# Kernel tuning notes

Hardware: AMD Instinct MI355X
Metric: run time of the kernel (lower is better)

Reference implementation:

```python
import jax, jax.numpy as jnp
import numpy as np

N = 50000          # num vertices
E = 20000          # num hyperedges
NNZ = 320000       # num incidences
IN_C = 256
HEADS = 8
OUT_C = 32
D = HEADS * OUT_C  # 256, projected feature dim


def setup_inputs() -> dict:
    key = jax.random.key(0)
    k1, k2, k3, k4 = jax.random.split(key, 4)
    X = jax.random.normal(k1, (N, IN_C), dtype=jnp.float32)
    vertex = jax.random.randint(k2, (NNZ,), 0, N, dtype=jnp.int64)
    edges = jax.random.randint(k3, (NNZ,), 0, E, dtype=jnp.int64)
    # Linear weight stored as [in, out] so projection is X @ W
    W = jax.random.normal(k4, (IN_C, D), dtype=jnp.float32) / np.sqrt(IN_C)
    eps = jnp.zeros((1,), dtype=jnp.float32)
    return {"X": X, "vertex": vertex, "edges": edges, "W": W, "eps": eps}


def reference(X, vertex, edges, W, eps):
    # Linear projection: [N, in] @ [in, heads*out] -> [N, D]
    Xp = X @ W
    # vertex -> edge: gather per-incidence vertex features, sum into hyperedges
    Xve = Xp[vertex]                                            # [NNZ, D]
    Xe = jax.ops.segment_sum(Xve, edges, num_segments=E)        # [E, D]
    # edge -> vertex: gather per-incidence edge features, sum into vertices
    Xev = Xe[edges]                                             # [NNZ, D]
    Xv = jax.ops.segment_sum(Xev, vertex, num_segments=N)       # [N, D]
    # GIN update
    return (1.0 + eps) * Xp + Xv
```

## Files before the change

kernel.cpp:

```cpp
#include <hip/hip_runtime.h>

constexpr int NV   = 50000;
constexpr int NE   = 20000;
constexpr int NNZI = 320000;
constexpr int KD   = 256;
constexpr int DD   = 256;
constexpr int ECAP = 64;
constexpr int VCAP = 32;

constexpr size_t alignup256(size_t x) { return (x + 255) & ~(size_t)255; }

constexpr size_t XPH_BYTES   = (size_t)NV * DD * 2;
constexpr size_t XEH_BYTES   = (size_t)NE * DD * 2;
constexpr size_t DEGV_BYTES  = alignup256((size_t)NV * sizeof(int));
constexpr size_t DEGE_BYTES  = alignup256((size_t)NE * sizeof(int));
constexpr size_t VLIST_BYTES = (size_t)NV * VCAP * sizeof(int);
constexpr size_t ELIST_BYTES = (size_t)NE * ECAP * sizeof(int);
constexpr size_t BPACK_ELEMS = 8ull * 16 * 64 * 8;
constexpr size_t BPACK_BYTES = BPACK_ELEMS * 2;

constexpr size_t XPH_OFF   = 0;
constexpr size_t XEH_OFF   = XPH_OFF + XPH_BYTES;
constexpr size_t DEGV_OFF  = XEH_OFF + XEH_BYTES;
constexpr size_t DEGE_OFF  = DEGV_OFF + DEGV_BYTES;
constexpr size_t VLIST_OFF = DEGE_OFF + DEGE_BYTES;
constexpr size_t ELIST_OFF = VLIST_OFF + VLIST_BYTES;
constexpr size_t BF_OFF    = ELIST_OFF + ELIST_BYTES;

typedef float    floatx4 __attribute__((ext_vector_type(4)));
typedef _Float16 halfx8  __attribute__((ext_vector_type(8)));
typedef _Float16 halfx4  __attribute__((ext_vector_type(4)));

__global__ __launch_bounds__(256) void pack_w(
        const float* __restrict__ W, _Float16* __restrict__ Bf) {
    const int idx  = blockIdx.x * 256 + threadIdx.x;
    const int k0   = idx >> 10;
    const int nt   = (idx >> 6) & 15;
    const int lane = idx & 63;
    const int krow = k0 * 32 + ((lane >> 4) << 3);
    const int ncol = nt * 16 + (lane & 15);
#pragma unroll
    for (int j = 0; j < 8; ++j)
        Bf[(size_t)idx * 8 + j] = (_Float16)W[(size_t)(krow + j) * DD + ncol];
}

__global__ __launch_bounds__(256) void gemm_mfma(
        const float* __restrict__ X, const _Float16* __restrict__ Bf,
        _Float16* __restrict__ Xp_h) {
    const int lane = threadIdx.x & 63;
    const int wv   = threadIdx.x >> 6;
    const int row_base = blockIdx.x * 64 + (wv >> 1) * 32;
    const int ntg0     = blockIdx.y * 8 + (wv & 1) * 4;

    floatx4 acc[2][4];
#pragma unroll
    for (int mt = 0; mt < 2; ++mt)
#pragma unroll
        for (int nt = 0; nt < 4; ++nt) acc[mt][nt] = (floatx4)0.f;

    const int lrow   = lane & 15;
    const int kgroup = (lane >> 4) << 3;

    int r0 = row_base + lrow;       if (r0 >= NV) r0 = NV - 1;
    int r1 = row_base + 16 + lrow;  if (r1 >= NV) r1 = NV - 1;
    const float* pA0 = &X[(size_t)r0 * KD + kgroup];
    const float* pA1 = &X[(size_t)r1 * KD + kgroup];

    float4 xb[2][2][2];
    halfx8 bb[2][4];

    auto loads = [&](int k0, int buf) {
        xb[buf][0][0] = *reinterpret_cast<const float4*>(pA0 + k0 * 32);
        xb[buf][0][1] = *reinterpret_cast<const float4*>(pA0 + k0 * 32 + 4);
        xb[buf][1][0] = *reinterpret_cast<const float4*>(pA1 + k0 * 32);
        xb[buf][1][1] = *reinterpret_cast<const float4*>(pA1 + k0 * 32 + 4);
#pragma unroll
        for (int nt = 0; nt < 4; ++nt) {
            const size_t boff = ((size_t)(k0 * 16 + ntg0 + nt) * 64 + lane) * 8;
            bb[buf][nt] = *reinterpret_cast<const halfx8*>(&Bf[boff]);
        }
    };

    loads(0, 0);
    for (int k0 = 0; k0 < 8; ++k0) {
        const int cur = k0 & 1;
        if (k0 < 7) loads(k0 + 1, cur ^ 1);
        halfx8 a[2];
#pragma unroll
        for (int mt = 0; mt < 2; ++mt) {
            const float* xp = reinterpret_cast<const float*>(&xb[cur][mt][0]);
#pragma unroll
            for (int j = 0; j < 8; ++j) a[mt][j] = (_Float16)xp[j];
        }
#pragma unroll
        for (int nt = 0; nt < 4; ++nt)
#pragma unroll
            for (int mt = 0; mt < 2; ++mt)
                acc[mt][nt] = __builtin_amdgcn_mfma_f32_16x16x32_f16(a[mt], bb[cur][nt], acc[mt][nt], 0, 0, 0);
    }

    const int rgroup = (lane >> 4) << 2;
#pragma unroll
    for (int mt = 0; mt < 2; ++mt) {
#pragma unroll
        for (int r = 0; r < 4; ++r) {
            const int row = row_base + mt * 16 + rgroup + r;
            if (row < NV) {
#pragma unroll
                for (int nt = 0; nt < 4; ++nt)
                    Xp_h[(size_t)row * DD + (ntg0 + nt) * 16 + (lane & 15)] =
                        (_Float16)acc[mt][nt][r];
            }
        }
    }
}

__global__ __launch_bounds__(256) void build_csr(
        const int* __restrict__ vertex, const int* __restrict__ edges,
        int* __restrict__ deg_v, int* __restrict__ deg_e,
        int* __restrict__ vlist, int* __restrict__ elist) {
    const int i = blockIdx.x * blockDim.x + threadIdx.x;
    if (i >= NNZI) return;
    const int v = vertex[i];
    const int e = edges[i];
    const int pe = atomicAdd(&deg_e[e], 1);
    if (pe < ECAP) elist[(size_t)e * ECAP + pe] = v;
    const int pv = atomicAdd(&deg_v[v], 1);
    if (pv < VCAP) vlist[(size_t)v * VCAP + pv] = e;
}

__global__ __launch_bounds__(256) void edge_gather(
        const _Float16* __restrict__ Xp_h, const int* __restrict__ deg_e,
        const int* __restrict__ elist, _Float16* __restrict__ Xe_h) {
    const int lane = threadIdx.x & 63;
    const int wid  = (blockIdx.x * blockDim.x + threadIdx.x) >> 6;
    if (wid >= NE) return;
    int cnt = deg_e[wid];
    if (cnt > ECAP) cnt = ECAP;
    const int idxl = elist[(size_t)wid * ECAP + lane];
    const int col  = lane * 4;
    float a0 = 0.f, a1 = 0.f, a2 = 0.f, a3 = 0.f;
    for (int base = 0; base < cnt; base += 8) {
#pragma unroll
        for (int jj = 0; jj < 8; ++jj) {
            const int j   = base + jj;
            const int sel = j < cnt ? j : 0;
            const float s = j < cnt ? 1.f : 0.f;
            const int v = __shfl(idxl, sel);
            const halfx4 x = *reinterpret_cast<const halfx4*>(&Xp_h[(size_t)v * DD + col]);
            a0 = fmaf(s, (float)x[0], a0);
            a1 = fmaf(s, (float)x[1], a1);
            a2 = fmaf(s, (float)x[2], a2);
            a3 = fmaf(s, (float)x[3], a3);
        }
    }
    halfx4 o;
    o[0] = (_Float16)a0; o[1] = (_Float16)a1; o[2] = (_Float16)a2; o[3] = (_Float16)a3;
    *reinterpret_cast<halfx4*>(&Xe_h[(size_t)wid * DD + col]) = o;
}

__global__ __launch_bounds__(256) void vertex_gather(
        const _Float16* __restrict__ Xp_h, const _Float16* __restrict__ Xe_h,
        const int* __restrict__ deg_v, const int* __restrict__ vlist,
        const float* __restrict__ eps, float* __restrict__ out) {
    const int lane = threadIdx.x & 63;
    const int wid  = (blockIdx.x * blockDim.x + threadIdx.x) >> 6;
    if (wid >= NV) return;
    int cnt = deg_v[wid];
    if (cnt > VCAP) cnt = VCAP;
    const int idxl = vlist[(size_t)wid * VCAP + lane];
    const int col  = lane * 4;
    const float e1 = 1.0f + eps[0];
    const halfx4 xp = *reinterpret_cast<const halfx4*>(&Xp_h[(size_t)wid * DD + col]);
    float a0 = e1 * (float)xp[0], a1 = e1 * (float)xp[1];
    float a2 = e1 * (float)xp[2], a3 = e1 * (float)xp[3];
    for (int base = 0; base < cnt; base += 8) {
#pragma unroll
        for (int jj = 0; jj < 8; ++jj) {
            const int j   = base + jj;
            const int sel = j < cnt ? j : 0;
            const float s = j < cnt ? 1.f : 0.f;
            const int e = __shfl(idxl, sel);
            const halfx4 t = *reinterpret_cast<const halfx4*>(&Xe_h[(size_t)e * DD + col]);
            a0 = fmaf(s, (float)t[0], a0);
            a1 = fmaf(s, (float)t[1], a1);
            a2 = fmaf(s, (float)t[2], a2);
            a3 = fmaf(s, (float)t[3], a3);
        }
    }
    float4 o; o.x = a0; o.y = a1; o.z = a2; o.w = a3;
    *reinterpret_cast<float4*>(&out[(size_t)wid * DD + col]) = o;
}

extern "C" void kernel_launch(void* const* d_in, const int* in_sizes, int n_in,
                              void* d_out, int out_size, void* d_ws, size_t ws_size,
                              hipStream_t stream) {
    const float* X      = (const float*)d_in[0];
    const int*   vertex = (const int*)d_in[1];
    const int*   edges  = (const int*)d_in[2];
    const float* W      = (const float*)d_in[3];
    const float* eps    = (const float*)d_in[4];
    float* out = (float*)d_out;
    char*  ws  = (char*)d_ws;

    _Float16* Xp_h = (_Float16*)(ws + XPH_OFF);
    _Float16* Xe_h = (_Float16*)(ws + XEH_OFF);
    int*   deg_v = (int*)(ws + DEGV_OFF);
    int*   deg_e = (int*)(ws + DEGE_OFF);
    int*   vlist = (int*)(ws + VLIST_OFF);
    int*   elist = (int*)(ws + ELIST_OFF);
    _Float16* Bf  = (_Float16*)(ws + BF_OFF);

    hipMemsetAsync(ws + DEGV_OFF, 0, DEGV_BYTES + DEGE_BYTES, stream);

    pack_w<<<32, 256, 0, stream>>>(W, Bf);
    gemm_mfma<<<dim3((NV + 63) / 64, 2), 256, 0, stream>>>(X, Bf, Xp_h);
    build_csr<<<(NNZI + 255) / 256, 256, 0, stream>>>(vertex, edges, deg_v, deg_e, vlist, elist);
    edge_gather<<<(NE + 3) / 4, 256, 0, stream>>>(Xp_h, deg_e, elist, Xe_h);
    vertex_gather<<<(NV + 3) / 4, 256, 0, stream>>>(Xp_h, Xe_h, deg_v, vlist, eps, out);
}
```

Measured before the change: 217.3 us.

## Fuse X fp16 cast, W packing and CSR build into one prep kernel

Adds a prep kernel that converts X to fp16 in a separate buffer, packs W, and builds the incidence lists, replacing three launches with one. The GEMM now reads fp16 X directly, which halves its A-operand traffic and removes the in-loop conversion. The GEMM also gets an occupancy hint in its launch bounds. The cost is an extra full pass over X (read fp32, write fp16, read back fp16), which may cost more than the GEMM savings.

```diff
diff --git a/kernel.cpp b/kernel.cpp
--- a/kernel.cpp
+++ b/kernel.cpp
@@ -12,6 +12,7 @@
 
 constexpr size_t XPH_BYTES   = (size_t)NV * DD * 2;
 constexpr size_t XEH_BYTES   = (size_t)NE * DD * 2;
+constexpr size_t XH_BYTES    = (size_t)NV * KD * 2;
 constexpr size_t DEGV_BYTES  = alignup256((size_t)NV * sizeof(int));
 constexpr size_t DEGE_BYTES  = alignup256((size_t)NE * sizeof(int));
 constexpr size_t VLIST_BYTES = (size_t)NV * VCAP * sizeof(int);
@@ -21,7 +22,8 @@
 
 constexpr size_t XPH_OFF   = 0;
 constexpr size_t XEH_OFF   = XPH_OFF + XPH_BYTES;
-constexpr size_t DEGV_OFF  = XEH_OFF + XEH_BYTES;
+constexpr size_t XH_OFF    = XEH_OFF + XEH_BYTES;
+constexpr size_t DEGV_OFF  = XH_OFF + XH_BYTES;
 constexpr size_t DEGE_OFF  = DEGV_OFF + DEGV_BYTES;
 constexpr size_t VLIST_OFF = DEGE_OFF + DEGE_BYTES;
 constexpr size_t ELIST_OFF = VLIST_OFF + VLIST_BYTES;
@@ -31,21 +33,56 @@
 typedef _Float16 halfx8  __attribute__((ext_vector_type(8)));
 typedef _Float16 halfx4  __attribute__((ext_vector_type(4)));
 
-__global__ __launch_bounds__(256) void pack_w(
-        const float* __restrict__ W, _Float16* __restrict__ Bf) {
-    const int idx  = blockIdx.x * 256 + threadIdx.x;
-    const int k0   = idx >> 10;
-    const int nt   = (idx >> 6) & 15;
-    const int lane = idx & 63;
-    const int krow = k0 * 32 + ((lane >> 4) << 3);
-    const int ncol = nt * 16 + (lane & 15);
-#pragma unroll
-    for (int j = 0; j < 8; ++j)
-        Bf[(size_t)idx * 8 + j] = (_Float16)W[(size_t)(krow + j) * DD + ncol];
-}
-
-__global__ __launch_bounds__(256) void gemm_mfma(
-        const float* __restrict__ X, const _Float16* __restrict__ Bf,
+constexpr int CAST_BLOCKS = 1024;
+constexpr int PACK_BLOCKS = 32;
+constexpr int CSR_BLOCKS  = (NNZI + 255) / 256;
+constexpr int PREP_BLOCKS = CAST_BLOCKS + PACK_BLOCKS + CSR_BLOCKS;
+
+__global__ __launch_bounds__(256) void fused_prep(
+        const float* __restrict__ X, const float* __restrict__ W,
+        const int* __restrict__ vertex, const int* __restrict__ edges,
+        _Float16* __restrict__ X_h, _Float16* __restrict__ Bf,
+        int* __restrict__ deg_v, int* __restrict__ deg_e,
+        int* __restrict__ vlist, int* __restrict__ elist) {
+    const int b = blockIdx.x;
+    if (b < CAST_BLOCKS) {
+        constexpr int NCHUNK = NV * KD / 8;
+        const int tid = b * 256 + threadIdx.x;
+        for (int c = tid; c < NCHUNK; c += CAST_BLOCKS * 256) {
+            const float4 lo = *reinterpret_cast<const float4*>(&X[(size_t)c * 8]);
+            const float4 hi = *reinterpret_cast<const float4*>(&X[(size_t)c * 8 + 4]);
+            halfx8 h;
+            h[0] = (_Float16)lo.x; h[1] = (_Float16)lo.y;
+            h[2] = (_Float16)lo.z; h[3] = (_Float16)lo.w;
+            h[4] = (_Float16)hi.x; h[5] = (_Float16)hi.y;
+            h[6] = (_Float16)hi.z; h[7] = (_Float16)hi.w;
+            *reinterpret_cast<halfx8*>(&X_h[(size_t)c * 8]) = h;
+        }
+    } else if (b < CAST_BLOCKS + PACK_BLOCKS) {
+        const int idx  = (b - CAST_BLOCKS) * 256 + threadIdx.x;
+        const int k0   = idx >> 10;
+        const int nt   = (idx >> 6) & 15;
+        const int lane = idx & 63;
+        const int krow = k0 * 32 + ((lane >> 4) << 3);
+        const int ncol = nt * 16 + (lane & 15);
+#pragma unroll
+        for (int j = 0; j < 8; ++j)
+            Bf[(size_t)idx * 8 + j] = (_Float16)W[(size_t)(krow + j) * DD + ncol];
+    } else {
+        const int i = (b - CAST_BLOCKS - PACK_BLOCKS) * 256 + threadIdx.x;
+        if (i < NNZI) {
+            const int v = vertex[i];
+            const int e = edges[i];
+            const int pe = atomicAdd(&deg_e[e], 1);
+            if (pe < ECAP) elist[(size_t)e * ECAP + pe] = v;
+            const int pv = atomicAdd(&deg_v[v], 1);
+            if (pv < VCAP) vlist[(size_t)v * VCAP + pv] = e;
+        }
+    }
+}
+
+__global__ __launch_bounds__(256, 4) void gemm_mfma(
+        const _Float16* __restrict__ X_h, const _Float16* __restrict__ Bf,
         _Float16* __restrict__ Xp_h) {
     const int lane = threadIdx.x & 63;
     const int wv   = threadIdx.x >> 6;
@@ -63,17 +100,15 @@
 
     int r0 = row_base + lrow;       if (r0 >= NV) r0 = NV - 1;
     int r1 = row_base + 16 + lrow;  if (r1 >= NV) r1 = NV - 1;
-    const float* pA0 = &X[(size_t)r0 * KD + kgroup];
-    const float* pA1 = &X[(size_t)r1 * KD + kgroup];
-
-    float4 xb[2][2][2];
+    const _Float16* pA0 = &X_h[(size_t)r0 * KD + kgroup];
+    const _Float16* pA1 = &X_h[(size_t)r1 * KD + kgroup];
+
+    halfx8 ab[2][2];
     halfx8 bb[2][4];
 
     auto loads = [&](int k0, int buf) {
-        xb[buf][0][0] = *reinterpret_cast<const float4*>(pA0 + k0 * 32);
-        xb[buf][0][1] = *reinterpret_cast<const float4*>(pA0 + k0 * 32 + 4);
-        xb[buf][1][0] = *reinterpret_cast<const float4*>(pA1 + k0 * 32);
-        xb[buf][1][1] = *reinterpret_cast<const float4*>(pA1 + k0 * 32 + 4);
+        ab[buf][0] = *reinterpret_cast<const halfx8*>(pA0 + k0 * 32);
+        ab[buf][1] = *reinterpret_cast<const halfx8*>(pA1 + k0 * 32);
 #pragma unroll
         for (int nt = 0; nt < 4; ++nt) {
             const size_t boff = ((size_t)(k0 * 16 + ntg0 + nt) * 64 + lane) * 8;
@@ -85,18 +120,12 @@
     for (int k0 = 0; k0 < 8; ++k0) {
         const int cur = k0 & 1;
         if (k0 < 7) loads(k0 + 1, cur ^ 1);
-        halfx8 a[2];
-#pragma unroll
-        for (int mt = 0; mt < 2; ++mt) {
-            const float* xp = reinterpret_cast<const float*>(&xb[cur][mt][0]);
-#pragma unroll
-            for (int j = 0; j < 8; ++j) a[mt][j] = (_Float16)xp[j];
-        }
 #pragma unroll
         for (int nt = 0; nt < 4; ++nt)
 #pragma unroll
             for (int mt = 0; mt < 2; ++mt)
-                acc[mt][nt] = __builtin_amdgcn_mfma_f32_16x16x32_f16(a[mt], bb[cur][nt], acc[mt][nt], 0, 0, 0);
+                acc[mt][nt] = __builtin_amdgcn_mfma_f32_16x16x32_f16(
+                    ab[cur][mt], bb[cur][nt], acc[mt][nt], 0, 0, 0);
     }
 
     const int rgroup = (lane >> 4) << 2;
@@ -113,20 +142,6 @@
             }
         }
     }
-}
-
-__global__ __launch_bounds__(256) void build_csr(
-        const int* __restrict__ vertex, const int* __restrict__ edges,
-        int* __restrict__ deg_v, int* __restrict__ deg_e,
-        int* __restrict__ vlist, int* __restrict__ elist) {
-    const int i = blockIdx.x * blockDim.x + threadIdx.x;
-    if (i >= NNZI) return;
-    const int v = vertex[i];
-    const int e = edges[i];
-    const int pe = atomicAdd(&deg_e[e], 1);
-    if (pe < ECAP) elist[(size_t)e * ECAP + pe] = v;
-    const int pv = atomicAdd(&deg_v[v], 1);
-    if (pv < VCAP) vlist[(size_t)v * VCAP + pv] = e;
 }
 
 __global__ __launch_bounds__(256) void edge_gather(
@@ -205,6 +220,7 @@
 
     _Float16* Xp_h = (_Float16*)(ws + XPH_OFF);
     _Float16* Xe_h = (_Float16*)(ws + XEH_OFF);
+    _Float16* X_h  = (_Float16*)(ws + XH_OFF);
     int*   deg_v = (int*)(ws + DEGV_OFF);
     int*   deg_e = (int*)(ws + DEGE_OFF);
     int*   vlist = (int*)(ws + VLIST_OFF);
@@ -213,9 +229,9 @@
 
     hipMemsetAsync(ws + DEGV_OFF, 0, DEGV_BYTES + DEGE_BYTES, stream);
 
-    pack_w<<<32, 256, 0, stream>>>(W, Bf);
-    gemm_mfma<<<dim3((NV + 63) / 64, 2), 256, 0, stream>>>(X, Bf, Xp_h);
-    build_csr<<<(NNZI + 255) / 256, 256, 0, stream>>>(vertex, edges, deg_v, deg_e, vlist, elist);
+    fused_prep<<<PREP_BLOCKS, 256, 0, stream>>>(
+        X, W, vertex, edges, X_h, Bf, deg_v, deg_e, vlist, elist);
+    gemm_mfma<<<dim3((NV + 63) / 64, 2), 256, 0, stream>>>(X_h, Bf, Xp_h);
     edge_gather<<<(NE + 3) / 4, 256, 0, stream>>>(Xp_h, deg_e, elist, Xe_h);
     vertex_gather<<<(NV + 3) / 4, 256, 0, stream>>>(Xp_h, Xe_h, deg_v, vlist, eps, out);
 }
```

Result: no change. 215.5 us (-0.8%).
